# Kernel optimization log

Measured on AMD Instinct MI355X. Metric: run time of the kernel, lower is better.

The kernel has to match this reference:

```python
import jax, jax.numpy as jnp
import numpy as np

N_NODES = 50000
BN_EPS = 1e-5


def setup_inputs() -> dict:
    key = jax.random.key(0)
    ks = jax.random.split(key, 16)
    N, IN, H, OUT, E = N_NODES, 512, 128, 64, 800000
    s = lambda fi, fo: 1.0 / np.sqrt(fi)
    inp = {
        'x': jax.random.normal(ks[0], (N, IN), dtype=jnp.float32),
        'edge_index': jax.random.randint(ks[1], (2, E), 0, N, dtype=jnp.int32),
        # mlpA: Linear(N -> H)
        'WA': jax.random.uniform(ks[2], (H, N), jnp.float32, -s(N, H), s(N, H)),
        'bA': jax.random.uniform(ks[3], (H,), jnp.float32, -s(N, H), s(N, H)),
        # mlpX: Linear(IN -> H)
        'WX': jax.random.uniform(ks[4], (H, IN), jnp.float32, -s(IN, H), s(IN, H)),
        'bX': jax.random.uniform(ks[5], (H,), jnp.float32, -s(IN, H), s(IN, H)),
        # W: Linear(2H -> H)
        'W': jax.random.uniform(ks[6], (H, 2 * H), jnp.float32, -s(2 * H, H), s(2 * H, H)),
        'bW': jax.random.uniform(ks[7], (H,), jnp.float32, -s(2 * H, H), s(2 * H, H)),
        # mlp_final layer 1: Linear(H -> H) + BN
        'Wf1': jax.random.uniform(ks[8], (H, H), jnp.float32, -s(H, H), s(H, H)),
        'bf1': jax.random.uniform(ks[9], (H,), jnp.float32, -s(H, H), s(H, H)),
        'gamma': jnp.ones((H,), jnp.float32),
        'beta': jnp.zeros((H,), jnp.float32),
        # mlp_final layer 2: Linear(H -> OUT)
        'Wf2': jax.random.uniform(ks[10], (OUT, H), jnp.float32, -s(H, OUT), s(H, OUT)),
        'bf2': jax.random.uniform(ks[11], (OUT,), jnp.float32, -s(H, OUT), s(H, OUT)),
    }
    return inp


def _batchnorm(x, gamma, beta):
    # training-mode BN over the node/batch axis (biased variance, as in torch)
    mean = jnp.mean(x, axis=0)
    var = jnp.var(x, axis=0)
    return (x - mean) * jax.lax.rsqrt(var + BN_EPS) * gamma + beta


def reference(x, edge_index, WA, bA, WX, bX, W, bW, Wf1, bf1, gamma, beta, Wf2, bf2):
    row, col = edge_index[0], edge_index[1]
    row = row - row.min()
    # xA = A @ WA.T + bA  where A[i,j]=1 per (row,col) edge (duplicates sum).
    # Equivalent SpMM: gather columns of WA at `col`, segment-sum into `row`.
    xA = jax.ops.segment_sum(WA.T[col], row, num_segments=N_NODES) + bA  # [N, H]
    xX = x @ WX.T + bX  # [N, H]
    h = jnp.concatenate([xA, xX], axis=-1) @ W.T + bW  # [N, H]
    h = jax.nn.relu(h + xA + xX)
    # mlp_final (num_layers=2): Linear -> ReLU -> BN -> (dropout off) -> Linear
    h = jax.nn.relu(h @ Wf1.T + bf1)
    h = _batchnorm(h, gamma, beta)
    out = h @ Wf2.T + bf2  # [N, OUT]
    return out
```

## Files before the change

kernel.cpp:

```cpp
#include <hip/hip_runtime.h>

typedef __bf16 bf16_t;
typedef __bf16 bf16x8 __attribute__((ext_vector_type(8)));
typedef float f32x4 __attribute__((ext_vector_type(4)));

#define IN_DIM 512
#define H_DIM 128
#define OUT_DIM 64
#define BN_EPS 1e-5f
#define SCAN_BLK 2048

#define MFMA(a, b, c) __builtin_amdgcn_mfma_f32_16x16x32_bf16(a, b, c, 0, 0, 0)

__device__ __forceinline__ float ld_adapt(const void* p, size_t i, int isbf) {
    return isbf ? (float)((const bf16_t*)p)[i] : ((const float*)p)[i];
}

__device__ __forceinline__ void split8(const float* p, bf16x8& hi, bf16x8& lo) {
    f32x4 v0 = *(const f32x4*)p;
    f32x4 v1 = *(const f32x4*)(p + 4);
#pragma unroll
    for (int i = 0; i < 8; ++i) {
        float f = (i < 4) ? v0[i] : v1[i - 4];
        bf16_t h = (bf16_t)f;
        hi[i] = h;
        lo[i] = (bf16_t)(f - (float)h);
    }
}

__global__ void k_init(const void* bA, const void* bX, const void* bW, const void* bf1,
                       const void* gamma, const void* beta, const void* bf2,
                       float* __restrict__ dst, int* __restrict__ flag) {
    __shared__ int s_isbf;
    if (threadIdx.x == 0) {
        unsigned u = *(const unsigned*)gamma;
        int f = (u == 0x3F803F80u) ? 1 : 0;
        *flag = f;
        s_isbf = f;
    }
    __syncthreads();
    int isbf = s_isbf;
    int t = threadIdx.x;
    dst[t] = ld_adapt(bA, t, isbf);
    dst[128 + t] = ld_adapt(bX, t, isbf);
    dst[256 + t] = ld_adapt(bW, t, isbf);
    dst[384 + t] = ld_adapt(bf1, t, isbf);
    dst[512 + t] = ld_adapt(gamma, t, isbf);
    dst[640 + t] = ld_adapt(beta, t, isbf);
    if (t < OUT_DIM) dst[768 + t] = ld_adapt(bf2, t, isbf);
}

__global__ __launch_bounds__(256) void k_transpose(const void* __restrict__ WA,
                                                   float* __restrict__ WAT, int N,
                                                   const int* __restrict__ flag) {
    __shared__ float t[64][130];
    int isbf = *flag;
    int n0 = blockIdx.x * 64;
    int tid = threadIdx.x;
#pragma unroll
    for (int i = 0; i < 32; ++i) {
        int lin = i * 256 + tid;
        int h = lin >> 6, nl = lin & 63;
        int n = n0 + nl;
        t[nl][h] = (n < N) ? ld_adapt(WA, (size_t)h * N + n, isbf) : 0.f;
    }
    __syncthreads();
#pragma unroll
    for (int i = 0; i < 32; ++i) {
        int lin = i * 256 + tid;
        int nl = lin >> 7, h = lin & 127;
        int n = n0 + nl;
        if (n < N) WAT[(size_t)n * H_DIM + h] = t[nl][h];
    }
}

__global__ __launch_bounds__(256) void k_prep(const int* __restrict__ rows, int E,
                                              int* __restrict__ bmin, int* __restrict__ cnt,
                                              int* __restrict__ rank) {
    __shared__ int sm[4];
    int i = blockIdx.x * 256 + threadIdx.x;
    int m = 0x7fffffff;
    if (i < E) {
        int r = rows[i];
        m = r;
        rank[i] = atomicAdd(&cnt[r], 1);
    }
    for (int off = 32; off; off >>= 1) m = min(m, __shfl_xor(m, off, 64));
    if ((threadIdx.x & 63) == 0) sm[threadIdx.x >> 6] = m;
    __syncthreads();
    if (threadIdx.x == 0)
        bmin[blockIdx.x] = min(min(sm[0], sm[1]), min(sm[2], sm[3]));
}

__global__ __launch_bounds__(256) void k_scan1(const int* __restrict__ cnt,
                                               int* __restrict__ offs,
                                               int* __restrict__ bsum, int N) {
    __shared__ int ts[256];
    int base = blockIdx.x * SCAN_BLK;
    int t = threadIdx.x;
    int v[8], s = 0;
#pragma unroll
    for (int i = 0; i < 8; ++i) {
        int idx = base + t * 8 + i;
        v[i] = (idx < N) ? cnt[idx] : 0;
        s += v[i];
    }
    ts[t] = s;
    __syncthreads();
    for (int off = 1; off < 256; off <<= 1) {
        int x = (t >= off) ? ts[t - off] : 0;
        __syncthreads();
        ts[t] += x;
        __syncthreads();
    }
    int run = ts[t] - s;
#pragma unroll
    for (int i = 0; i < 8; ++i) {
        int idx = base + t * 8 + i;
        if (idx < N) offs[idx] = run;
        run += v[i];
    }
    if (t == 255) bsum[blockIdx.x] = ts[255];
}

__global__ __launch_bounds__(256) void k_scan2(int* __restrict__ bsum, int* __restrict__ offs,
                                               int NB, int N, const int* __restrict__ bmin,
                                               int nbmin, int* __restrict__ minbuf) {
    __shared__ int sm[256];
    int t = threadIdx.x;
    int m = 0x7fffffff;
    for (int i = t; i < nbmin; i += 256) m = min(m, bmin[i]);
    sm[t] = m;
    __syncthreads();
    for (int off = 128; off; off >>= 1) {
        if (t < off) sm[t] = min(sm[t], sm[t + off]);
        __syncthreads();
    }
    if (t == 0) {
        *minbuf = sm[0];
        int run = 0;
        for (int b = 0; b < NB; ++b) {
            int v = bsum[b];
            bsum[b] = run;
            run += v;
        }
        offs[N] = run;
    }
}

__global__ __launch_bounds__(256) void k_scan3(int* __restrict__ offs, const int* __restrict__ bsum,
                                               int N) {
    int i = blockIdx.x * 256 + threadIdx.x;
    if (i >= N) return;
    offs[i] += bsum[i / SCAN_BLK];
}

__global__ __launch_bounds__(256) void k_build(const int* __restrict__ rows,
                                               const int* __restrict__ cols, int E,
                                               const int* __restrict__ offs,
                                               const int* __restrict__ rank,
                                               int* __restrict__ scol) {
    int i = blockIdx.x * 256 + threadIdx.x;
    if (i >= E) return;
    int r = rows[i];
    int pos = offs[r] + rank[i];
    scol[pos] = cols[i];
}

__global__ __launch_bounds__(256) void k_gather(const int* __restrict__ offs,
                                                const int* __restrict__ scol,
                                                const float* __restrict__ WAT,
                                                const float* __restrict__ bA_f,
                                                const int* __restrict__ minbuf,
                                                float* __restrict__ xA, int N) {
    int wave = threadIdx.x >> 6, lane = threadIdx.x & 63;
    int r = blockIdx.x * 4 + wave;
    if (r >= N) return;
    int b = r + *minbuf;
    int s = 0, e = 0;
    if (b < N) {
        s = offs[b];
        e = offs[b + 1];
    }
    float2 a0 = {0.f, 0.f}, a1 = {0.f, 0.f};
    int i = s;
    for (; i + 3 < e; i += 4) {
        int c0 = scol[i], c1 = scol[i + 1], c2 = scol[i + 2], c3 = scol[i + 3];
        float2 w0 = *(const float2*)(WAT + (size_t)c0 * H_DIM + lane * 2);
        float2 w1 = *(const float2*)(WAT + (size_t)c1 * H_DIM + lane * 2);
        float2 w2 = *(const float2*)(WAT + (size_t)c2 * H_DIM + lane * 2);
        float2 w3 = *(const float2*)(WAT + (size_t)c3 * H_DIM + lane * 2);
        a0.x += w0.x + w2.x; a0.y += w0.y + w2.y;
        a1.x += w1.x + w3.x; a1.y += w1.y + w3.y;
    }
    for (; i < e; ++i) {
        int c = scol[i];
        float2 w = *(const float2*)(WAT + (size_t)c * H_DIM + lane * 2);
        a0.x += w.x; a0.y += w.y;
    }
    float2 bias = *(const float2*)(bA_f + lane * 2);
    float2 out = {a0.x + a1.x + bias.x, a0.y + a1.y + bias.y};
    *(float2*)(xA + (size_t)r * H_DIM + lane * 2) = out;
}

__device__ __forceinline__ void pack_frag(const void* __restrict__ W, bf16_t* __restrict__ hi,
                                          bf16_t* __restrict__ lo, int K, int NC,
                                          int addres, int isbf, int f, int lane) {
    int ks = f / (NC >> 4), nt = f % (NC >> 4);
    int n = nt * 16 + (lane & 15);
    int k0 = ks * 32 + (lane >> 4) * 8;
    bf16_t* dh = hi + (size_t)f * 512 + lane * 8;
    bf16_t* dl = lo + (size_t)f * 512 + lane * 8;
#pragma unroll
    for (int j = 0; j < 8; ++j) {
        int kk = k0 + j;
        float v = ld_adapt(W, (size_t)n * K + kk, isbf);
        if (addres && (kk == n || kk == n + H_DIM)) v += 1.f;
        bf16_t h = (bf16_t)v;
        dh[j] = h;
        dl[j] = (bf16_t)(v - (float)h);
    }
}

__global__ __launch_bounds__(256) void k_pack3(const void* WX, bf16_t* WXh, bf16_t* WXl,
                                               const void* W, bf16_t* Wh, bf16_t* Wl,
                                               const void* Wf1, bf16_t* Wf1h, bf16_t* Wf1l,
                                               const int* __restrict__ flag) {
    int g = blockIdx.x * 256 + threadIdx.x;
    int f = g >> 6, lane = g & 63;
    int isbf = *flag;
    if (f < 128)
        pack_frag(WX, WXh, WXl, IN_DIM, H_DIM, 0, isbf, f, lane);
    else if (f < 192)
        pack_frag(W, Wh, Wl, 2 * H_DIM, H_DIM, 1, isbf, f - 128, lane);
    else if (f < 224)
        pack_frag(Wf1, Wf1h, Wf1l, H_DIM, H_DIM, 0, isbf, f - 192, lane);
}

__global__ __launch_bounds__(256) void k_fuseA(
    const void* __restrict__ x, const float* __restrict__ xAf,
    const bf16_t* __restrict__ WXh, const bf16_t* __restrict__ WXl,
    const bf16_t* __restrict__ Wh, const bf16_t* __restrict__ Wl,
    const bf16_t* __restrict__ Wf1h, const bf16_t* __restrict__ Wf1l,
    const float* __restrict__ smallf, float* __restrict__ h2,
    double* __restrict__ sums, double* __restrict__ sumsq,
    const int* __restrict__ flag, int M) {
    __shared__ float axx[4][16 * 132];
    __shared__ float ls_sum[H_DIM], ls_sq[H_DIM];
    int tid = threadIdx.x;
    int wave = tid >> 6, lane = tid & 63, l16 = lane & 15, quad = lane >> 4;
    int mbase = blockIdx.x * 64 + wave * 16;
    int isbf = *flag;
    float* ax = axx[wave];
    int r0 = min(mbase + l16, M - 1);
    const float* bX = smallf + 128;
    const float* bW = smallf + 256;
    const float* bf1 = smallf + 384;

    if (tid < H_DIM) {
        ls_sum[tid] = 0.f;
        ls_sq[tid] = 0.f;
    }
    __syncthreads();

    bf16x8 zero8;
#pragma unroll
    for (int i = 0; i < 8; ++i) zero8[i] = (bf16_t)0.f;

    f32x4 acc[8];
#pragma unroll
    for (int nt = 0; nt < 8; ++nt) acc[nt] = f32x4{0.f, 0.f, 0.f, 0.f};
    {
        size_t offx = (size_t)r0 * IN_DIM + quad * 8;
        for (int ks = 0; ks < 16; ++ks) {
            bf16x8 ah, al;
            if (isbf) {
                ah = *(const bf16x8*)((const bf16_t*)x + offx + ks * 32);
                al = zero8;
            } else {
                split8((const float*)x + offx + ks * 32, ah, al);
            }
            const bf16_t* bhp = WXh + (size_t)ks * 8 * 512 + lane * 8;
            const bf16_t* blp = WXl + (size_t)ks * 8 * 512 + lane * 8;
#pragma unroll
            for (int nt = 0; nt < 8; ++nt) {
                bf16x8 bh = *(const bf16x8*)(bhp + nt * 512);
                bf16x8 bl = *(const bf16x8*)(blp + nt * 512);
                acc[nt] = MFMA(ah, bh, acc[nt]);
                acc[nt] = MFMA(ah, bl, acc[nt]);
                acc[nt] = MFMA(al, bh, acc[nt]);
            }
        }
    }
#pragma unroll
    for (int nt = 0; nt < 8; ++nt) {
        int col = nt * 16 + l16;
        float b = bX[col];
#pragma unroll
        for (int r = 0; r < 4; ++r) {
            int lr = quad * 4 + r;
            ax[lr * 132 + col] = acc[nt][r] + b;
        }
    }

#pragma unroll
    for (int nt = 0; nt < 8; ++nt) acc[nt] = f32x4{0.f, 0.f, 0.f, 0.f};
    for (int ks = 0; ks < 8; ++ks) {
        bf16x8 ah, al;
        if (ks < 4)
            split8(xAf + (size_t)r0 * H_DIM + ks * 32 + quad * 8, ah, al);
        else
            split8(ax + l16 * 132 + (ks - 4) * 32 + quad * 8, ah, al);
        const bf16_t* bhp = Wh + (size_t)ks * 8 * 512 + lane * 8;
        const bf16_t* blp = Wl + (size_t)ks * 8 * 512 + lane * 8;
#pragma unroll
        for (int nt = 0; nt < 8; ++nt) {
            bf16x8 bh = *(const bf16x8*)(bhp + nt * 512);
            bf16x8 bl = *(const bf16x8*)(blp + nt * 512);
            acc[nt] = MFMA(ah, bh, acc[nt]);
            acc[nt] = MFMA(ah, bl, acc[nt]);
            acc[nt] = MFMA(al, bh, acc[nt]);
        }
    }
#pragma unroll
    for (int nt = 0; nt < 8; ++nt) {
        int col = nt * 16 + l16;
        float b = bW[col];
#pragma unroll
        for (int r = 0; r < 4; ++r) {
            int lr = quad * 4 + r;
            ax[lr * 132 + col] = fmaxf(acc[nt][r] + b, 0.f);
        }
    }

#pragma unroll
    for (int nt = 0; nt < 8; ++nt) acc[nt] = f32x4{0.f, 0.f, 0.f, 0.f};
    for (int ks = 0; ks < 4; ++ks) {
        bf16x8 ah, al;
        split8(ax + l16 * 132 + ks * 32 + quad * 8, ah, al);
        const bf16_t* bhp = Wf1h + (size_t)ks * 8 * 512 + lane * 8;
        const bf16_t* blp = Wf1l + (size_t)ks * 8 * 512 + lane * 8;
#pragma unroll
        for (int nt = 0; nt < 8; ++nt) {
            bf16x8 bh = *(const bf16x8*)(bhp + nt * 512);
            bf16x8 bl = *(const bf16x8*)(blp + nt * 512);
            acc[nt] = MFMA(ah, bh, acc[nt]);
            acc[nt] = MFMA(ah, bl, acc[nt]);
            acc[nt] = MFMA(al, bh, acc[nt]);
        }
    }
#pragma unroll
    for (int nt = 0; nt < 8; ++nt) {
        int col = nt * 16 + l16;
        float b = bf1[col];
        float s = 0.f, s2 = 0.f;
#pragma unroll
        for (int r = 0; r < 4; ++r) {
            int row = mbase + quad * 4 + r;
            if (row < M) {
                float v = fmaxf(acc[nt][r] + b, 0.f);
                h2[(size_t)row * H_DIM + col] = v;
                s += v;
                s2 += v * v;
            }
        }
        s += __shfl_xor(s, 16, 64);
        s += __shfl_xor(s, 32, 64);
        s2 += __shfl_xor(s2, 16, 64);
        s2 += __shfl_xor(s2, 32, 64);
        if (quad == 0) {
            atomicAdd(&ls_sum[col], s);
            atomicAdd(&ls_sq[col], s2);
        }
    }
    __syncthreads();
    if (tid < H_DIM) {
        atomicAdd(&sums[tid], (double)ls_sum[tid]);
        atomicAdd(&sumsq[tid], (double)ls_sq[tid]);
    }
}

__global__ __launch_bounds__(256) void k_packB(
    const void* __restrict__ Wf2, const float* __restrict__ smallf,
    const double* __restrict__ sums, const double* __restrict__ sumsq,
    bf16_t* __restrict__ W2h, bf16_t* __restrict__ W2l,
    float* __restrict__ b2g, const int* __restrict__ flag, int M) {
    __shared__ float aw[H_DIM], cw[H_DIM];
    int t = threadIdx.x;
    int isbf = *flag;
    const float* gamma_f = smallf + 512;
    const float* beta_f = smallf + 640;
    const float* bf2_f = smallf + 768;
    if (t < H_DIM) {
        double mean = sums[t] / (double)M;
        double var = sumsq[t] / (double)M - mean * mean;
        if (var < 0) var = 0;
        float a = gamma_f[t] * rsqrtf((float)var + BN_EPS);
        aw[t] = a;
        cw[t] = beta_f[t] - (float)mean * a;
    }
    __syncthreads();
    if (t < OUT_DIM) {
        float acc = bf2_f[t];
        for (int j = 0; j < H_DIM; ++j) acc += ld_adapt(Wf2, (size_t)t * H_DIM + j, isbf) * cw[j];
        b2g[t] = acc;
    }
    for (int u = t; u < 1024; u += 256) {
        int f = u >> 6, ln = u & 63;
        int ks = f >> 2, nt = f & 3;
        int n = nt * 16 + (ln & 15);
        int k0 = ks * 32 + (ln >> 4) * 8;
#pragma unroll
        for (int j = 0; j < 8; ++j) {
            float v = ld_adapt(Wf2, (size_t)n * H_DIM + k0 + j, isbf) * aw[k0 + j];
            bf16_t h = (bf16_t)v;
            W2h[f * 512 + ln * 8 + j] = h;
            W2l[f * 512 + ln * 8 + j] = (bf16_t)(v - (float)h);
        }
    }
}

__global__ __launch_bounds__(256) void k_fuseB(
    const float* __restrict__ h2, const bf16_t* __restrict__ W2h,
    const bf16_t* __restrict__ W2l, const float* __restrict__ b2g,
    void* __restrict__ outv, const int* __restrict__ flag, int M) {
    int t = threadIdx.x;
    int isbf = *flag;
    int wave = t >> 6, lane = t & 63, l16 = lane & 15, quad = lane >> 4;
    int mbase = blockIdx.x * 64 + wave * 16;
    int r0 = min(mbase + l16, M - 1);
    f32x4 acc4[4];
#pragma unroll
    for (int nt = 0; nt < 4; ++nt) acc4[nt] = f32x4{0.f, 0.f, 0.f, 0.f};
    for (int ks = 0; ks < 4; ++ks) {
        bf16x8 ah, al;
        split8(h2 + (size_t)r0 * H_DIM + ks * 32 + quad * 8, ah, al);
#pragma unroll
        for (int nt = 0; nt < 4; ++nt) {
            bf16x8 bh = *(const bf16x8*)(W2h + (ks * 4 + nt) * 512 + lane * 8);
            bf16x8 bl = *(const bf16x8*)(W2l + (ks * 4 + nt) * 512 + lane * 8);
            acc4[nt] = MFMA(ah, bh, acc4[nt]);
            acc4[nt] = MFMA(ah, bl, acc4[nt]);
            acc4[nt] = MFMA(al, bh, acc4[nt]);
        }
    }
#pragma unroll
    for (int nt = 0; nt < 4; ++nt) {
        int col = nt * 16 + l16;
        float b = b2g[col];
#pragma unroll
        for (int r = 0; r < 4; ++r) {
            int row = mbase + quad * 4 + r;
            if (row < M) {
                float v = acc4[nt][r] + b;
                if (isbf)
                    ((bf16_t*)outv)[(size_t)row * OUT_DIM + col] = (bf16_t)v;
                else
                    ((float*)outv)[(size_t)row * OUT_DIM + col] = v;
            }
        }
    }
}

extern "C" void kernel_launch(void* const* d_in, const int* in_sizes, int n_in,
                              void* d_out, int out_size, void* d_ws, size_t ws_size,
                              hipStream_t stream) {
    const void* x = d_in[0];
    const int* ei = (const int*)d_in[1];
    const void* WA = d_in[2];
    const void* bA = d_in[3];
    const void* WX = d_in[4];
    const void* bX = d_in[5];
    const void* W = d_in[6];
    const void* bW = d_in[7];
    const void* Wf1 = d_in[8];
    const void* bf1 = d_in[9];
    const void* gamma = d_in[10];
    const void* beta = d_in[11];
    const void* Wf2 = d_in[12];
    const void* bf2 = d_in[13];

    const int N = in_sizes[0] / IN_DIM;
    const int E = in_sizes[1] / 2;
    const int* rows = ei;
    const int* cols = ei + E;
    const int eblocks = (E + 255) / 256;

    char* ws = (char*)d_ws;
    size_t off = 0;
    auto alloc = [&](size_t bytes) {
        char* p = ws + off;
        off += (bytes + 255) & ~(size_t)255;
        return p;
    };
    int* flag = (int*)alloc(4);
    int* minbuf = (int*)alloc(4);
    float* smallf = (float*)alloc(832 * 4);
    double* sums = (double*)alloc(2 * H_DIM * 8);
    double* sumsq = sums + H_DIM;
    bf16_t* WXp_h = (bf16_t*)alloc((size_t)IN_DIM * H_DIM * 2);
    bf16_t* WXp_l = (bf16_t*)alloc((size_t)IN_DIM * H_DIM * 2);
    bf16_t* Wp_h = (bf16_t*)alloc((size_t)256 * H_DIM * 2);
    bf16_t* Wp_l = (bf16_t*)alloc((size_t)256 * H_DIM * 2);
    bf16_t* Wf1p_h = (bf16_t*)alloc((size_t)H_DIM * H_DIM * 2);
    bf16_t* Wf1p_l = (bf16_t*)alloc((size_t)H_DIM * H_DIM * 2);
    bf16_t* W2h = (bf16_t*)alloc((size_t)16 * 512 * 2);
    bf16_t* W2l = (bf16_t*)alloc((size_t)16 * 512 * 2);
    float* b2g = (float*)alloc(OUT_DIM * 4);
    int* cnt = (int*)alloc((size_t)N * 4);
    int* offs = (int*)alloc(((size_t)N + 1) * 4);
    int* rank = (int*)alloc((size_t)E * 4);
    int* bsum = (int*)alloc(64 * 4);
    int* bmin = (int*)alloc((size_t)eblocks * 4);
    int* scol = (int*)alloc((size_t)E * 4);
    float* WAT = (float*)alloc((size_t)N * H_DIM * 4);
    float* xAf = (float*)alloc((size_t)N * H_DIM * 4);
    float* h2 = WAT;

    float* bA_f = smallf + 0;

    hipMemsetAsync(cnt, 0, (size_t)N * 4, stream);
    hipMemsetAsync(sums, 0, 2 * H_DIM * 8, stream);

    k_init<<<1, 128, 0, stream>>>(bA, bX, bW, bf1, gamma, beta, bf2, smallf, flag);
    k_transpose<<<(N + 63) / 64, 256, 0, stream>>>(WA, WAT, N, flag);
    k_pack3<<<56, 256, 0, stream>>>(WX, WXp_h, WXp_l, W, Wp_h, Wp_l, Wf1, Wf1p_h, Wf1p_l, flag);

    k_prep<<<eblocks, 256, 0, stream>>>(rows, E, bmin, cnt, rank);
    int NB = (N + SCAN_BLK - 1) / SCAN_BLK;
    k_scan1<<<NB, 256, 0, stream>>>(cnt, offs, bsum, N);
    k_scan2<<<1, 256, 0, stream>>>(bsum, offs, NB, N, bmin, eblocks, minbuf);
    k_scan3<<<(N + 255) / 256, 256, 0, stream>>>(offs, bsum, N);
    k_build<<<eblocks, 256, 0, stream>>>(rows, cols, E, offs, rank, scol);
    k_gather<<<(N + 3) / 4, 256, 0, stream>>>(offs, scol, WAT, bA_f, minbuf, xAf, N);

    int fblocks = (N + 63) / 64;
    k_fuseA<<<fblocks, 256, 0, stream>>>(x, xAf, WXp_h, WXp_l, Wp_h, Wp_l, Wf1p_h, Wf1p_l,
                                         smallf, h2, sums, sumsq, flag, N);
    k_packB<<<1, 256, 0, stream>>>(Wf2, smallf, sums, sumsq, W2h, W2l, b2g, flag, N);
    k_fuseB<<<fblocks, 256, 0, stream>>>(h2, W2h, W2l, b2g, d_out, flag, N);
}
```

Baseline: 454.7 us.

## Add bf16-input fast paths: packed bf16 WA gather and reduced split MFMAs

When inputs are detected as bf16, the transposed WA is stored as packed bf16 pairs, halving the bytes the SpMM gather reads. The fused MLP kernel is templated on input type so the bf16 path drops the low-part MFMA terms for weights that are exact in bf16. The identity residual is then added in the epilogue instead of being folded into W. The fp32 path is unchanged apart from the compile-time specialization, which removes a runtime branch inside the loop.

```diff
diff --git a/kernel.cpp b/kernel.cpp
--- a/kernel.cpp
+++ b/kernel.cpp
@@ -26,6 +26,17 @@
         hi[i] = h;
         lo[i] = (bf16_t)(f - (float)h);
     }
+}
+
+__device__ __forceinline__ unsigned short bf16_bits(float f) {
+    bf16_t h = (bf16_t)f;
+    return __builtin_bit_cast(unsigned short, h);
+}
+
+__device__ __forceinline__ float2 bf2_unpack(unsigned v) {
+    bf16_t lo = __builtin_bit_cast(bf16_t, (unsigned short)(v & 0xffffu));
+    bf16_t hi = __builtin_bit_cast(bf16_t, (unsigned short)(v >> 16));
+    return float2{(float)lo, (float)hi};
 }
 
 __global__ void k_init(const void* bA, const void* bX, const void* bW, const void* bf1,
@@ -65,12 +76,26 @@
         t[nl][h] = (n < N) ? ld_adapt(WA, (size_t)h * N + n, isbf) : 0.f;
     }
     __syncthreads();
-#pragma unroll
-    for (int i = 0; i < 32; ++i) {
-        int lin = i * 256 + tid;
-        int nl = lin >> 7, h = lin & 127;
-        int n = n0 + nl;
-        if (n < N) WAT[(size_t)n * H_DIM + h] = t[nl][h];
+    if (isbf) {
+#pragma unroll
+        for (int i = 0; i < 16; ++i) {
+            int lin = i * 256 + tid;
+            int nl = lin >> 6, hp = lin & 63;
+            int n = n0 + nl;
+            if (n < N) {
+                unsigned u0 = bf16_bits(t[nl][hp * 2]);
+                unsigned u1 = bf16_bits(t[nl][hp * 2 + 1]);
+                ((unsigned*)WAT)[(size_t)n * 64 + hp] = u0 | (u1 << 16);
+            }
+        }
+    } else {
+#pragma unroll
+        for (int i = 0; i < 32; ++i) {
+            int lin = i * 256 + tid;
+            int nl = lin >> 7, h = lin & 127;
+            int n = n0 + nl;
+            if (n < N) WAT[(size_t)n * H_DIM + h] = t[nl][h];
+        }
     }
 }
 
@@ -172,11 +197,13 @@
                                                 const float* __restrict__ WAT,
                                                 const float* __restrict__ bA_f,
                                                 const int* __restrict__ minbuf,
+                                                const int* __restrict__ flag,
                                                 float* __restrict__ xA, int N) {
     int wave = threadIdx.x >> 6, lane = threadIdx.x & 63;
     int r = blockIdx.x * 4 + wave;
     if (r >= N) return;
     int b = r + *minbuf;
+    int isbf = *flag;
     int s = 0, e = 0;
     if (b < N) {
         s = offs[b];
@@ -184,19 +211,38 @@
     }
     float2 a0 = {0.f, 0.f}, a1 = {0.f, 0.f};
     int i = s;
-    for (; i + 3 < e; i += 4) {
-        int c0 = scol[i], c1 = scol[i + 1], c2 = scol[i + 2], c3 = scol[i + 3];
-        float2 w0 = *(const float2*)(WAT + (size_t)c0 * H_DIM + lane * 2);
-        float2 w1 = *(const float2*)(WAT + (size_t)c1 * H_DIM + lane * 2);
-        float2 w2 = *(const float2*)(WAT + (size_t)c2 * H_DIM + lane * 2);
-        float2 w3 = *(const float2*)(WAT + (size_t)c3 * H_DIM + lane * 2);
-        a0.x += w0.x + w2.x; a0.y += w0.y + w2.y;
-        a1.x += w1.x + w3.x; a1.y += w1.y + w3.y;
-    }
-    for (; i < e; ++i) {
-        int c = scol[i];
-        float2 w = *(const float2*)(WAT + (size_t)c * H_DIM + lane * 2);
-        a0.x += w.x; a0.y += w.y;
+    if (isbf) {
+        const unsigned* Wb = (const unsigned*)WAT;
+        for (; i + 3 < e; i += 4) {
+            int c0 = scol[i], c1 = scol[i + 1], c2 = scol[i + 2], c3 = scol[i + 3];
+            unsigned v0 = Wb[(size_t)c0 * 64 + lane];
+            unsigned v1 = Wb[(size_t)c1 * 64 + lane];
+            unsigned v2 = Wb[(size_t)c2 * 64 + lane];
+            unsigned v3 = Wb[(size_t)c3 * 64 + lane];
+            float2 w0 = bf2_unpack(v0), w1 = bf2_unpack(v1);
+            float2 w2 = bf2_unpack(v2), w3 = bf2_unpack(v3);
+            a0.x += w0.x + w2.x; a0.y += w0.y + w2.y;
+            a1.x += w1.x + w3.x; a1.y += w1.y + w3.y;
+        }
+        for (; i < e; ++i) {
+            float2 w = bf2_unpack(Wb[(size_t)scol[i] * 64 + lane]);
+            a0.x += w.x; a0.y += w.y;
+        }
+    } else {
+        for (; i + 3 < e; i += 4) {
+            int c0 = scol[i], c1 = scol[i + 1], c2 = scol[i + 2], c3 = scol[i + 3];
+            float2 w0 = *(const float2*)(WAT + (size_t)c0 * H_DIM + lane * 2);
+            float2 w1 = *(const float2*)(WAT + (size_t)c1 * H_DIM + lane * 2);
+            float2 w2 = *(const float2*)(WAT + (size_t)c2 * H_DIM + lane * 2);
+            float2 w3 = *(const float2*)(WAT + (size_t)c3 * H_DIM + lane * 2);
+            a0.x += w0.x + w2.x; a0.y += w0.y + w2.y;
+            a1.x += w1.x + w3.x; a1.y += w1.y + w3.y;
+        }
+        for (; i < e; ++i) {
+            int c = scol[i];
+            float2 w = *(const float2*)(WAT + (size_t)c * H_DIM + lane * 2);
+            a0.x += w.x; a0.y += w.y;
+        }
     }
     float2 bias = *(const float2*)(bA_f + lane * 2);
     float2 out = {a0.x + a1.x + bias.x, a0.y + a1.y + bias.y};
@@ -232,9 +278,172 @@
     if (f < 128)
         pack_frag(WX, WXh, WXl, IN_DIM, H_DIM, 0, isbf, f, lane);
     else if (f < 192)
-        pack_frag(W, Wh, Wl, 2 * H_DIM, H_DIM, 1, isbf, f - 128, lane);
+        pack_frag(W, Wh, Wl, 2 * H_DIM, H_DIM, isbf ? 0 : 1, isbf, f - 128, lane);
     else if (f < 224)
         pack_frag(Wf1, Wf1h, Wf1l, H_DIM, H_DIM, 0, isbf, f - 192, lane);
+}
+
+template <int ISBF>
+__device__ __forceinline__ void fuseA_body(
+    const void* __restrict__ x, const float* __restrict__ xAf,
+    const bf16_t* __restrict__ WXh, const bf16_t* __restrict__ WXl,
+    const bf16_t* __restrict__ Wh, const bf16_t* __restrict__ Wl,
+    const bf16_t* __restrict__ Wf1h, const bf16_t* __restrict__ Wf1l,
+    const float* __restrict__ smallf, float* __restrict__ h2, int M,
+    float* __restrict__ ax, float* __restrict__ ls_sum, float* __restrict__ ls_sq) {
+    int tid = threadIdx.x;
+    int wave = tid >> 6, lane = tid & 63, l16 = lane & 15, quad = lane >> 4;
+    int mbase = blockIdx.x * 64 + wave * 16;
+    int r0 = min(mbase + l16, M - 1);
+    const float* bX = smallf + 128;
+    const float* bW = smallf + 256;
+    const float* bf1 = smallf + 384;
+
+    f32x4 acc[8];
+#pragma unroll
+    for (int nt = 0; nt < 8; ++nt) acc[nt] = f32x4{0.f, 0.f, 0.f, 0.f};
+    if (ISBF) {
+        size_t offx = (size_t)r0 * IN_DIM + quad * 8;
+        for (int ks = 0; ks < 16; ++ks) {
+            bf16x8 ah = *(const bf16x8*)((const bf16_t*)x + offx + ks * 32);
+            const bf16_t* bhp = WXh + (size_t)ks * 8 * 512 + lane * 8;
+#pragma unroll
+            for (int nt = 0; nt < 8; ++nt) {
+                bf16x8 bh = *(const bf16x8*)(bhp + nt * 512);
+                acc[nt] = MFMA(ah, bh, acc[nt]);
+            }
+        }
+    } else {
+        size_t offx = (size_t)r0 * IN_DIM + quad * 8;
+        for (int ks = 0; ks < 16; ++ks) {
+            bf16x8 ah, al;
+            split8((const float*)x + offx + ks * 32, ah, al);
+            const bf16_t* bhp = WXh + (size_t)ks * 8 * 512 + lane * 8;
+            const bf16_t* blp = WXl + (size_t)ks * 8 * 512 + lane * 8;
+#pragma unroll
+            for (int nt = 0; nt < 8; ++nt) {
+                bf16x8 bh = *(const bf16x8*)(bhp + nt * 512);
+                bf16x8 bl = *(const bf16x8*)(blp + nt * 512);
+                acc[nt] = MFMA(ah, bh, acc[nt]);
+                acc[nt] = MFMA(ah, bl, acc[nt]);
+                acc[nt] = MFMA(al, bh, acc[nt]);
+            }
+        }
+    }
+#pragma unroll
+    for (int nt = 0; nt < 8; ++nt) {
+        int col = nt * 16 + l16;
+        float b = bX[col];
+#pragma unroll
+        for (int r = 0; r < 4; ++r) {
+            int lr = quad * 4 + r;
+            ax[lr * 132 + col] = acc[nt][r] + b;
+        }
+    }
+
+#pragma unroll
+    for (int nt = 0; nt < 8; ++nt) acc[nt] = f32x4{0.f, 0.f, 0.f, 0.f};
+    for (int ks = 0; ks < 8; ++ks) {
+        bf16x8 ah, al;
+        if (ks < 4)
+            split8(xAf + (size_t)r0 * H_DIM + ks * 32 + quad * 8, ah, al);
+        else
+            split8(ax + l16 * 132 + (ks - 4) * 32 + quad * 8, ah, al);
+        const bf16_t* bhp = Wh + (size_t)ks * 8 * 512 + lane * 8;
+        if (ISBF) {
+#pragma unroll
+            for (int nt = 0; nt < 8; ++nt) {
+                bf16x8 bh = *(const bf16x8*)(bhp + nt * 512);
+                acc[nt] = MFMA(ah, bh, acc[nt]);
+                acc[nt] = MFMA(al, bh, acc[nt]);
+            }
+        } else {
+            const bf16_t* blp = Wl + (size_t)ks * 8 * 512 + lane * 8;
+#pragma unroll
+            for (int nt = 0; nt < 8; ++nt) {
+                bf16x8 bh = *(const bf16x8*)(bhp + nt * 512);
+                bf16x8 bl = *(const bf16x8*)(blp + nt * 512);
+                acc[nt] = MFMA(ah, bh, acc[nt]);
+                acc[nt] = MFMA(ah, bl, acc[nt]);
+                acc[nt] = MFMA(al, bh, acc[nt]);
+            }
+        }
+    }
+    if (ISBF) {
+#pragma unroll
+        for (int nt = 0; nt < 8; ++nt) {
+            int col = nt * 16 + l16;
+            float b = bW[col];
+#pragma unroll
+            for (int r = 0; r < 4; ++r) {
+                int lr = quad * 4 + r;
+                int rr = min(mbase + lr, M - 1);
+                float resid = xAf[(size_t)rr * H_DIM + col] + ax[lr * 132 + col];
+                ax[lr * 132 + col] = fmaxf(acc[nt][r] + b + resid, 0.f);
+            }
+        }
+    } else {
+#pragma unroll
+        for (int nt = 0; nt < 8; ++nt) {
+            int col = nt * 16 + l16;
+            float b = bW[col];
+#pragma unroll
+            for (int r = 0; r < 4; ++r) {
+                int lr = quad * 4 + r;
+                ax[lr * 132 + col] = fmaxf(acc[nt][r] + b, 0.f);
+            }
+        }
+    }
+
+#pragma unroll
+    for (int nt = 0; nt < 8; ++nt) acc[nt] = f32x4{0.f, 0.f, 0.f, 0.f};
+    for (int ks = 0; ks < 4; ++ks) {
+        bf16x8 ah, al;
+        split8(ax + l16 * 132 + ks * 32 + quad * 8, ah, al);
+        const bf16_t* bhp = Wf1h + (size_t)ks * 8 * 512 + lane * 8;
+        if (ISBF) {
+#pragma unroll
+            for (int nt = 0; nt < 8; ++nt) {
+                bf16x8 bh = *(const bf16x8*)(bhp + nt * 512);
+                acc[nt] = MFMA(ah, bh, acc[nt]);
+                acc[nt] = MFMA(al, bh, acc[nt]);
+            }
+        } else {
+            const bf16_t* blp = Wf1l + (size_t)ks * 8 * 512 + lane * 8;
+#pragma unroll
+            for (int nt = 0; nt < 8; ++nt) {
+                bf16x8 bh = *(const bf16x8*)(bhp + nt * 512);
+                bf16x8 bl = *(const bf16x8*)(blp + nt * 512);
+                acc[nt] = MFMA(ah, bh, acc[nt]);
+                acc[nt] = MFMA(ah, bl, acc[nt]);
+                acc[nt] = MFMA(al, bh, acc[nt]);
+            }
+        }
+    }
+#pragma unroll
+    for (int nt = 0; nt < 8; ++nt) {
+        int col = nt * 16 + l16;
+        float b = bf1[col];
+        float s = 0.f, s2 = 0.f;
+#pragma unroll
+        for (int r = 0; r < 4; ++r) {
+            int row = mbase + quad * 4 + r;
+            if (row < M) {
+                float v = fmaxf(acc[nt][r] + b, 0.f);
+                h2[(size_t)row * H_DIM + col] = v;
+                s += v;
+                s2 += v * v;
+            }
+        }
+        s += __shfl_xor(s, 16, 64);
+        s += __shfl_xor(s, 32, 64);
+        s2 += __shfl_xor(s2, 16, 64);
+        s2 += __shfl_xor(s2, 32, 64);
+        if (quad == 0) {
+            atomicAdd(&ls_sum[col], s);
+            atomicAdd(&ls_sq[col], s2);
+        }
+    }
 }
 
 __global__ __launch_bounds__(256) void k_fuseA(
@@ -248,131 +457,16 @@
     __shared__ float axx[4][16 * 132];
     __shared__ float ls_sum[H_DIM], ls_sq[H_DIM];
     int tid = threadIdx.x;
-    int wave = tid >> 6, lane = tid & 63, l16 = lane & 15, quad = lane >> 4;
-    int mbase = blockIdx.x * 64 + wave * 16;
-    int isbf = *flag;
-    float* ax = axx[wave];
-    int r0 = min(mbase + l16, M - 1);
-    const float* bX = smallf + 128;
-    const float* bW = smallf + 256;
-    const float* bf1 = smallf + 384;
-
     if (tid < H_DIM) {
         ls_sum[tid] = 0.f;
         ls_sq[tid] = 0.f;
     }
     __syncthreads();
-
-    bf16x8 zero8;
-#pragma unroll
-    for (int i = 0; i < 8; ++i) zero8[i] = (bf16_t)0.f;
-
-    f32x4 acc[8];
-#pragma unroll
-    for (int nt = 0; nt < 8; ++nt) acc[nt] = f32x4{0.f, 0.f, 0.f, 0.f};
-    {
-        size_t offx = (size_t)r0 * IN_DIM + quad * 8;
-        for (int ks = 0; ks < 16; ++ks) {
-            bf16x8 ah, al;
-            if (isbf) {
-                ah = *(const bf16x8*)((const bf16_t*)x + offx + ks * 32);
-                al = zero8;
-            } else {
-                split8((const float*)x + offx + ks * 32, ah, al);
-            }
-            const bf16_t* bhp = WXh + (size_t)ks * 8 * 512 + lane * 8;
-            const bf16_t* blp = WXl + (size_t)ks * 8 * 512 + lane * 8;
-#pragma unroll
-            for (int nt = 0; nt < 8; ++nt) {
-                bf16x8 bh = *(const bf16x8*)(bhp + nt * 512);
-                bf16x8 bl = *(const bf16x8*)(blp + nt * 512);
-                acc[nt] = MFMA(ah, bh, acc[nt]);
-                acc[nt] = MFMA(ah, bl, acc[nt]);
-                acc[nt] = MFMA(al, bh, acc[nt]);
-            }
-        }
-    }
-#pragma unroll
-    for (int nt = 0; nt < 8; ++nt) {
-        int col = nt * 16 + l16;
-        float b = bX[col];
-#pragma unroll
-        for (int r = 0; r < 4; ++r) {
-            int lr = quad * 4 + r;
-            ax[lr * 132 + col] = acc[nt][r] + b;
-        }
-    }
-
-#pragma unroll
-    for (int nt = 0; nt < 8; ++nt) acc[nt] = f32x4{0.f, 0.f, 0.f, 0.f};
-    for (int ks = 0; ks < 8; ++ks) {
-        bf16x8 ah, al;
-        if (ks < 4)
-            split8(xAf + (size_t)r0 * H_DIM + ks * 32 + quad * 8, ah, al);
-        else
-            split8(ax + l16 * 132 + (ks - 4) * 32 + quad * 8, ah, al);
-        const bf16_t* bhp = Wh + (size_t)ks * 8 * 512 + lane * 8;
-        const bf16_t* blp = Wl + (size_t)ks * 8 * 512 + lane * 8;
-#pragma unroll
-        for (int nt = 0; nt < 8; ++nt) {
-            bf16x8 bh = *(const bf16x8*)(bhp + nt * 512);
-            bf16x8 bl = *(const bf16x8*)(blp + nt * 512);
-            acc[nt] = MFMA(ah, bh, acc[nt]);
-            acc[nt] = MFMA(ah, bl, acc[nt]);
-            acc[nt] = MFMA(al, bh, acc[nt]);
-        }
-    }
-#pragma unroll
-    for (int nt = 0; nt < 8; ++nt) {
-        int col = nt * 16 + l16;
-        float b = bW[col];
-#pragma unroll
-        for (int r = 0; r < 4; ++r) {
-            int lr = quad * 4 + r;
-            ax[lr * 132 + col] = fmaxf(acc[nt][r] + b, 0.f);
-        }
-    }
-
-#pragma unroll
-    for (int nt = 0; nt < 8; ++nt) acc[nt] = f32x4{0.f, 0.f, 0.f, 0.f};
-    for (int ks = 0; ks < 4; ++ks) {
-        bf16x8 ah, al;
-        split8(ax + l16 * 132 + ks * 32 + quad * 8, ah, al);
-        const bf16_t* bhp = Wf1h + (size_t)ks * 8 * 512 + lane * 8;
-        const bf16_t* blp = Wf1l + (size_t)ks * 8 * 512 + lane * 8;
-#pragma unroll
-        for (int nt = 0; nt < 8; ++nt) {
-            bf16x8 bh = *(const bf16x8*)(bhp + nt * 512);
-            bf16x8 bl = *(const bf16x8*)(blp + nt * 512);
-            acc[nt] = MFMA(ah, bh, acc[nt]);
-            acc[nt] = MFMA(ah, bl, acc[nt]);
-            acc[nt] = MFMA(al, bh, acc[nt]);
-        }
-    }
-#pragma unroll
-    for (int nt = 0; nt < 8; ++nt) {
-        int col = nt * 16 + l16;
-        float b = bf1[col];
-        float s = 0.f, s2 = 0.f;
-#pragma unroll
-        for (int r = 0; r < 4; ++r) {
-            int row = mbase + quad * 4 + r;
-            if (row < M) {
-                float v = fmaxf(acc[nt][r] + b, 0.f);
-                h2[(size_t)row * H_DIM + col] = v;
-                s += v;
-                s2 += v * v;
-            }
-        }
-        s += __shfl_xor(s, 16, 64);
-        s += __shfl_xor(s, 32, 64);
-        s2 += __shfl_xor(s2, 16, 64);
-        s2 += __shfl_xor(s2, 32, 64);
-        if (quad == 0) {
-            atomicAdd(&ls_sum[col], s);
-            atomicAdd(&ls_sq[col], s2);
-        }
-    }
+    float* ax = axx[tid >> 6];
+    if (*flag)
+        fuseA_body<1>(x, xAf, WXh, WXl, Wh, Wl, Wf1h, Wf1l, smallf, h2, M, ax, ls_sum, ls_sq);
+    else
+        fuseA_body<0>(x, xAf, WXh, WXl, Wh, Wl, Wf1h, Wf1l, smallf, h2, M, ax, ls_sum, ls_sq);
     __syncthreads();
     if (tid < H_DIM) {
         atomicAdd(&sums[tid], (double)ls_sum[tid]);
@@ -532,7 +626,7 @@
     k_scan2<<<1, 256, 0, stream>>>(bsum, offs, NB, N, bmin, eblocks, minbuf);
     k_scan3<<<(N + 255) / 256, 256, 0, stream>>>(offs, bsum, N);
     k_build<<<eblocks, 256, 0, stream>>>(rows, cols, E, offs, rank, scol);
-    k_gather<<<(N + 3) / 4, 256, 0, stream>>>(offs, scol, WAT, bA_f, minbuf, xAf, N);
+    k_gather<<<(N + 3) / 4, 256, 0, stream>>>(offs, scol, WAT, bA_f, minbuf, flag, xAf, N);
 
     int fblocks = (N + 63) / 64;
     k_fuseA<<<fblocks, 256, 0, stream>>>(x, xAf, WXp_h, WXp_l, Wp_h, Wp_l, Wf1p_h, Wf1p_l,
```

New measurement: 457.2 us. About the same (+0.6%).
